# Kernel optimization log

Hardware: AMD Instinct MI355X
Metric: run time of the kernel (lower is better)

Reference implementation:

```python
import jax, jax.numpy as jnp
import numpy as np

N_NODES = 100000
IN_DIM, HID_DIM, OUT_DIM = 1433, 16, 7
N_EDGES = 3200000


def gcn_conv(x, edge_index, W, b, num_nodes):
    # add self loops
    loop = jnp.arange(num_nodes, dtype=edge_index.dtype)
    src = jnp.concatenate([edge_index[0], loop])  # [E+N]
    dst = jnp.concatenate([edge_index[1], loop])
    h = x @ W + b  # [N, out]
    # degree computed on row (edge_index[0]) as in the torch code
    deg = jax.ops.segment_sum(jnp.ones_like(src, dtype=h.dtype), src,
                              num_segments=num_nodes)
    dis = deg ** -0.5  # self-loops guarantee deg >= 1
    norm = dis[src] * dis[dst]  # [E+N]
    msg = norm[:, None] * h[src]  # gather + scale
    return jax.ops.segment_sum(msg, dst, num_segments=num_nodes)  # scatter-add


def setup_inputs() -> dict:
    key = jax.random.key(0)
    k1, k2, k3, k4, k5, k6 = jax.random.split(key, 6)
    x = jax.random.normal(k1, (N_NODES, IN_DIM), dtype=jnp.float32)
    edge_index = jax.random.randint(k2, (2, N_EDGES), 0, N_NODES, dtype=jnp.int64)
    s1 = 1.0 / np.sqrt(IN_DIM)
    s2 = 1.0 / np.sqrt(HID_DIM)
    W1 = jax.random.uniform(k3, (IN_DIM, HID_DIM), jnp.float32, -s1, s1)
    b1 = jax.random.uniform(k4, (HID_DIM,), jnp.float32, -s1, s1)
    W2 = jax.random.uniform(k5, (HID_DIM, OUT_DIM), jnp.float32, -s2, s2)
    b2 = jax.random.uniform(k6, (OUT_DIM,), jnp.float32, -s2, s2)
    return {"x": x, "edge_index": edge_index, "W1": W1, "b1": b1,
            "W2": W2, "b2": b2}


def reference(x, edge_index, W1, b1, W2, b2):
    n = x.shape[0]
    h = gcn_conv(x, edge_index, W1, b1, n)
    h = jax.nn.relu(h)
    # dropout is inactive in eval mode (training=False)
    h = gcn_conv(h, edge_index, W2, b2, n)
    return jax.nn.log_softmax(h, axis=1)
```

## Files before the change

### kernel.cpp

```cpp
#include <hip/hip_runtime.h>
#include <math.h>

constexpr int IN_DIM = 1433;
constexpr int HID    = 16;
constexpr int OUTD   = 7;

__device__ __forceinline__ int edge_get(const int* __restrict__ ei, long long idx, int is64) {
    return is64 ? ei[2 * idx] : ei[idx];
}

__global__ void k_detect_init(const int* __restrict__ ei, int* __restrict__ flag,
                              int* __restrict__ deg, int* __restrict__ cnt, int n) {
    int i = blockIdx.x * blockDim.x + threadIdx.x;
    if (i < n) { deg[i] = 1; cnt[i] = 0; }
    if (blockIdx.x == 0) {
        __shared__ int nzsh;
        if (threadIdx.x == 0) nzsh = 0;
        __syncthreads();
        int nz = 0;
        for (int j = threadIdx.x; j < 2048; j += blockDim.x)
            nz |= (ei[2 * j + 1] != 0) ? 1 : 0;
        if (nz) nzsh = 1;
        __syncthreads();
        if (threadIdx.x == 0) *flag = (nzsh == 0) ? 1 : 0;
    }
}

__global__ __launch_bounds__(128) void k_gemm1h(
        const float* __restrict__ x, const float* __restrict__ W1,
        const float* __restrict__ b1, float* __restrict__ h1, int n,
        const int* __restrict__ ei, int E, const int* __restrict__ flag,
        int* __restrict__ deg, int* __restrict__ cnt, int* __restrict__ packed,
        int nHist) {
    if ((int)blockIdx.x < nHist) {
        int is64 = *flag;
        long long stride = (long long)nHist * blockDim.x;
        for (long long e = (long long)blockIdx.x * blockDim.x + threadIdx.x;
             e < E; e += stride) {
            int s = edge_get(ei, e, is64);
            int d = edge_get(ei, (long long)E + e, is64);
            atomicAdd(&deg[s], 1);
            int slot = atomicAdd(&cnt[d], 1);
            packed[e] = (d << 14) | (slot & 16383);
        }
        return;
    }

    constexpr int BK = 32, XST = 36;
    __shared__ __align__(16) float xs[128 * XST];
    __shared__ __align__(16) float wsm[BK * HID];
    const int t    = threadIdx.x;
    const int c4   = t & 3;
    const int rq   = t >> 2;
    const int row0 = ((int)blockIdx.x - nHist) * 128;

    float xreg[32];
    float wreg[4];
    float4 acc[4];
    #pragma unroll
    for (int j = 0; j < 4; ++j) acc[j] = make_float4(0.f, 0.f, 0.f, 0.f);

    auto issue = [&](int kt) {
        #pragma unroll
        for (int i = 0; i < 32; ++i) {
            int idx  = t + 128 * i;
            int srow = idx >> 5;
            int scol = idx & 31;
            int gr   = row0 + srow;
            int col  = kt + scol;
            float v = 0.f;
            if (gr < n && col < IN_DIM) v = x[(long long)gr * IN_DIM + col];
            xreg[i] = v;
        }
        #pragma unroll
        for (int u = 0; u < 4; ++u) {
            int idx = t + 128 * u;
            int kk  = idx >> 4;
            wreg[u] = (kt + kk < IN_DIM) ? W1[(kt + kk) * HID + (idx & 15)] : 0.f;
        }
    };
    auto commit = [&]() {
        #pragma unroll
        for (int i = 0; i < 32; ++i) {
            int idx  = t + 128 * i;
            int srow = idx >> 5;
            int scol = idx & 31;
            xs[srow * XST + scol] = xreg[i];
        }
        #pragma unroll
        for (int u = 0; u < 4; ++u) wsm[t + 128 * u] = wreg[u];
    };

    const int nkt = (IN_DIM + BK - 1) / BK;
    issue(0);
    for (int it = 0; it < nkt; ++it) {
        commit();
        __syncthreads();
        if (it + 1 < nkt) issue((it + 1) * BK);
        #pragma unroll
        for (int k4 = 0; k4 < BK / 4; ++k4) {
            int k = k4 * 4;
            float4 w0 = *(const float4*)&wsm[(k + 0) * HID + c4 * 4];
            float4 w1 = *(const float4*)&wsm[(k + 1) * HID + c4 * 4];
            float4 w2 = *(const float4*)&wsm[(k + 2) * HID + c4 * 4];
            float4 w3 = *(const float4*)&wsm[(k + 3) * HID + c4 * 4];
            #pragma unroll
            for (int j = 0; j < 4; ++j) {
                float4 xv = *(const float4*)&xs[(rq + 32 * j) * XST + k];
                acc[j].x += xv.x * w0.x + xv.y * w1.x + xv.z * w2.x + xv.w * w3.x;
                acc[j].y += xv.x * w0.y + xv.y * w1.y + xv.z * w2.y + xv.w * w3.y;
                acc[j].z += xv.x * w0.z + xv.y * w1.z + xv.z * w2.z + xv.w * w3.z;
                acc[j].w += xv.x * w0.w + xv.y * w1.w + xv.z * w2.w + xv.w * w3.w;
            }
        }
        __syncthreads();
    }

    float4 bv = *(const float4*)&b1[c4 * 4];
    #pragma unroll
    for (int j = 0; j < 4; ++j) {
        int gr = row0 + rq + 32 * j;
        if (gr < n) {
            float4 hv;
            hv.x = acc[j].x + bv.x;
            hv.y = acc[j].y + bv.y;
            hv.z = acc[j].z + bv.z;
            hv.w = acc[j].w + bv.w;
            *(float4*)&h1[(long long)gr * HID + c4 * 4] = hv;
        }
    }
}

__global__ __launch_bounds__(256) void k_scan1(const int* __restrict__ cnt,
                                               int* __restrict__ bsum,
                                               float* __restrict__ dis, int n) {
    __shared__ int sh[256];
    int t = threadIdx.x;
    int base = blockIdx.x * 1024 + t * 4;
    int s = 0;
    #pragma unroll
    for (int j = 0; j < 4; ++j) {
        int i = base + j;
        if (i < n) {
            s += cnt[i];
            int v = ((const int*)dis)[i];
            dis[i] = rsqrtf((float)v);
        }
    }
    sh[t] = s; __syncthreads();
    for (int o = 128; o > 0; o >>= 1) {
        if (t < o) sh[t] += sh[t + o];
        __syncthreads();
    }
    if (t == 0) bsum[blockIdx.x] = sh[0];
}

__global__ __launch_bounds__(256) void k_scan2(const int* __restrict__ bsum,
                                               int* __restrict__ boff,
                                               int* __restrict__ rp,
                                               int nb, int n, int E) {
    __shared__ int sh[256];
    int t = threadIdx.x;
    int v = (t < nb) ? bsum[t] : 0;
    sh[t] = v; __syncthreads();
    for (int o = 1; o < 256; o <<= 1) {
        int tmp = (t >= o) ? sh[t - o] : 0;
        __syncthreads();
        sh[t] += tmp;
        __syncthreads();
    }
    boff[t] = sh[t] - v;
    if (t == 0) rp[n] = E;
}

__global__ __launch_bounds__(256) void k_scan3(const int* __restrict__ cnt,
                                               const int* __restrict__ boff,
                                               int* __restrict__ rp, int n) {
    __shared__ int sh[256];
    int t = threadIdx.x;
    int base = blockIdx.x * 1024 + t * 4;
    int c[4];
    int s = 0;
    #pragma unroll
    for (int j = 0; j < 4; ++j) {
        int i = base + j;
        c[j] = (i < n) ? cnt[i] : 0;
        s += c[j];
    }
    sh[t] = s; __syncthreads();
    for (int o = 1; o < 256; o <<= 1) {
        int tmp = (t >= o) ? sh[t - o] : 0;
        __syncthreads();
        sh[t] += tmp;
        __syncthreads();
    }
    int run = boff[blockIdx.x] + sh[t] - s;
    #pragma unroll
    for (int j = 0; j < 4; ++j) {
        int i = base + j;
        if (i < n) rp[i] = run;
        run += c[j];
    }
}

__global__ void k_place(const int* __restrict__ ei, int E, const int* __restrict__ flag,
                        const int* __restrict__ packed, const int* __restrict__ rp,
                        int* __restrict__ csr) {
    int e = blockIdx.x * blockDim.x + threadIdx.x;
    if (e >= E) return;
    int is64 = *flag;
    int s  = edge_get(ei, e, is64);
    int p  = packed[e];
    int d  = p >> 14;
    int sl = p & 16383;
    csr[rp[d] + sl] = s;
}

__global__ void k_scale(const float* __restrict__ dis, const float* __restrict__ in,
                        float* __restrict__ out, int n, int squared) {
    int i = blockIdx.x * blockDim.x + threadIdx.x;
    if (i >= n * 4) return;
    int row = i >> 2;
    float d = dis[row];
    if (squared) d *= d;
    float4 v = *(const float4*)&in[(long long)i * 4];
    v.x *= d; v.y *= d; v.z *= d; v.w *= d;
    *(float4*)&out[(long long)i * 4] = v;
}

__global__ __launch_bounds__(256) void k_gather1f(
        const int* __restrict__ rp, const int* __restrict__ csr,
        const float* __restrict__ dis, const float* __restrict__ hs1,
        const float* __restrict__ W2, const float* __restrict__ b2,
        float* __restrict__ hs2, int n) {
    __shared__ float w2s[HID * OUTD];
    __shared__ float b2s[OUTD];
    int t = threadIdx.x;
    if (t < HID * OUTD) w2s[t] = W2[t];
    if (t < OUTD) b2s[t] = b2[t];
    __syncthreads();

    int tid  = blockIdx.x * blockDim.x + t;
    int node = tid >> 2;
    int q    = tid & 3;
    if (node >= n) return;

    float4 acc = *(const float4*)&hs1[(long long)node * HID + q * 4];

    int i = rp[node], end = rp[node + 1];
    for (; i + 4 <= end; i += 4) {
        int s0 = csr[i], s1 = csr[i + 1], s2 = csr[i + 2], s3 = csr[i + 3];
        float4 h0 = *(const float4*)&hs1[(long long)s0 * HID + q * 4];
        float4 h1 = *(const float4*)&hs1[(long long)s1 * HID + q * 4];
        float4 h2 = *(const float4*)&hs1[(long long)s2 * HID + q * 4];
        float4 h3 = *(const float4*)&hs1[(long long)s3 * HID + q * 4];
        acc.x += (h0.x + h1.x) + (h2.x + h3.x);
        acc.y += (h0.y + h1.y) + (h2.y + h3.y);
        acc.z += (h0.z + h1.z) + (h2.z + h3.z);
        acc.w += (h0.w + h1.w) + (h2.w + h3.w);
    }
    for (; i < end; ++i) {
        int s = csr[i];
        float4 h = *(const float4*)&hs1[(long long)s * HID + q * 4];
        acc.x += h.x; acc.y += h.y; acc.z += h.z; acc.w += h.w;
    }

    float dn = dis[node];
    float r0 = fmaxf(dn * acc.x, 0.f), r1 = fmaxf(dn * acc.y, 0.f);
    float r2 = fmaxf(dn * acc.z, 0.f), r3 = fmaxf(dn * acc.w, 0.f);
    float p[OUTD];
    #pragma unroll
    for (int j = 0; j < OUTD; ++j) {
        p[j] = r0 * w2s[(q * 4 + 0) * OUTD + j]
             + r1 * w2s[(q * 4 + 1) * OUTD + j]
             + r2 * w2s[(q * 4 + 2) * OUTD + j]
             + r3 * w2s[(q * 4 + 3) * OUTD + j];
    }
    #pragma unroll
    for (int j = 0; j < OUTD; ++j) {
        p[j] += __shfl_xor(p[j], 1, 4);
        p[j] += __shfl_xor(p[j], 2, 4);
    }
    hs2[(long long)node * OUTD + q] = dn * (p[q] + b2s[q]);
    if (q < 3) hs2[(long long)node * OUTD + q + 4] = dn * (p[q + 4] + b2s[q + 4]);
}

__global__ __launch_bounds__(256) void k_gather2(
        const int* __restrict__ rp, const int* __restrict__ csr,
        const float* __restrict__ dis, const float* __restrict__ hs2,
        float* __restrict__ out, int n) {
    int t = threadIdx.x;
    int node = blockIdx.x * 32 + (t >> 3);
    int q = t & 7;
    if (node >= n) return;
    float acc = -1e30f;
    if (q < OUTD) {
        acc = hs2[(long long)node * OUTD + q];
        int i = rp[node], end = rp[node + 1];
        for (; i + 8 <= end; i += 8) {
            int s0 = csr[i],     s1 = csr[i + 1], s2 = csr[i + 2], s3 = csr[i + 3];
            int s4 = csr[i + 4], s5 = csr[i + 5], s6 = csr[i + 6], s7 = csr[i + 7];
            float v0 = hs2[(long long)s0 * OUTD + q];
            float v1 = hs2[(long long)s1 * OUTD + q];
            float v2 = hs2[(long long)s2 * OUTD + q];
            float v3 = hs2[(long long)s3 * OUTD + q];
            float v4 = hs2[(long long)s4 * OUTD + q];
            float v5 = hs2[(long long)s5 * OUTD + q];
            float v6 = hs2[(long long)s6 * OUTD + q];
            float v7 = hs2[(long long)s7 * OUTD + q];
            acc += ((v0 + v1) + (v2 + v3)) + ((v4 + v5) + (v6 + v7));
        }
        for (; i < end; ++i) {
            int s = csr[i];
            acc += hs2[(long long)s * OUTD + q];
        }
        acc *= dis[node];
    }
    float m = acc;
    #pragma unroll
    for (int o = 1; o < 8; o <<= 1) m = fmaxf(m, __shfl_xor(m, o, 8));
    float ex = (q < OUTD) ? expf(acc - m) : 0.f;
    float ss = ex;
    #pragma unroll
    for (int o = 1; o < 8; o <<= 1) ss += __shfl_xor(ss, o, 8);
    if (q < OUTD) out[(long long)node * OUTD + q] = acc - m - logf(ss);
}

__global__ void k_detect(const int* __restrict__ ei, int* __restrict__ flag) {
    __shared__ int nzsh;
    if (threadIdx.x == 0) nzsh = 0;
    __syncthreads();
    int nz = 0;
    for (int i = threadIdx.x; i < 2048; i += blockDim.x)
        nz |= (ei[2 * i + 1] != 0) ? 1 : 0;
    if (nz) nzsh = 1;
    __syncthreads();
    if (threadIdx.x == 0) *flag = (nzsh == 0) ? 1 : 0;
}

__global__ void k_deg_init(int* __restrict__ deg, int n) {
    int i = blockIdx.x * blockDim.x + threadIdx.x;
    if (i < n) deg[i] = 1;
}

__global__ void k_deg_count(const int* __restrict__ ei, int E,
                            const int* __restrict__ flag, int* __restrict__ deg) {
    int e = blockIdx.x * blockDim.x + threadIdx.x;
    if (e >= E) return;
    int is64 = *flag;
    int s = edge_get(ei, e, is64);
    atomicAdd(&deg[s], 1);
}

__global__ void k_deg_finish(float* __restrict__ dis, int n) {
    int i = blockIdx.x * blockDim.x + threadIdx.x;
    if (i < n) {
        int v = ((const int*)dis)[i];
        dis[i] = rsqrtf((float)v);
    }
}

__global__ void k_agg1(const int* __restrict__ ei, int E, const int* __restrict__ flag,
                       const float* __restrict__ dis, const float* __restrict__ h1,
                       float* __restrict__ a1) {
    long long tid = (long long)blockIdx.x * blockDim.x + threadIdx.x;
    int e = (int)(tid >> 2);
    int q = (int)(tid & 3);
    if (e >= E) return;
    int is64 = *flag;
    int s = edge_get(ei, e, is64);
    int d = edge_get(ei, (long long)E + e, is64);
    float nrm = dis[s] * dis[d];
    float4 v = *(const float4*)&h1[(long long)s * HID + q * 4];
    float* o = &a1[(long long)d * HID + q * 4];
    atomicAdd(o + 0, nrm * v.x);
    atomicAdd(o + 1, nrm * v.y);
    atomicAdd(o + 2, nrm * v.z);
    atomicAdd(o + 3, nrm * v.w);
}

__global__ __launch_bounds__(256) void k_gemm2(
        const float* __restrict__ a1, const float* __restrict__ W2,
        const float* __restrict__ b2, const float* __restrict__ dis,
        float* __restrict__ h2, float* __restrict__ a2, int n) {
    __shared__ float w2s[HID * OUTD];
    __shared__ float b2s[OUTD];
    int t = threadIdx.x;
    if (t < HID * OUTD) w2s[t] = W2[t];
    if (t < OUTD) b2s[t] = b2[t];
    __syncthreads();
    int r = blockIdx.x * blockDim.x + t;
    if (r >= n) return;
    float a[16];
    #pragma unroll
    for (int i = 0; i < 4; ++i) {
        float4 v = *(const float4*)&a1[(long long)r * HID + i * 4];
        a[4 * i + 0] = fmaxf(v.x, 0.f);
        a[4 * i + 1] = fmaxf(v.y, 0.f);
        a[4 * i + 2] = fmaxf(v.z, 0.f);
        a[4 * i + 3] = fmaxf(v.w, 0.f);
    }
    float dd = 0.f;
    if (a2) { float d = dis[r]; dd = d * d; }
    #pragma unroll
    for (int j = 0; j < OUTD; ++j) {
        float acc = b2s[j];
        #pragma unroll
        for (int k = 0; k < HID; ++k) acc += a[k] * w2s[k * OUTD + j];
        h2[(long long)r * OUTD + j] = acc;
        if (a2) a2[(long long)r * OUTD + j] = dd * acc;
    }
}

__global__ void k_agg2(const int* __restrict__ ei, int E, const int* __restrict__ flag,
                       const float* __restrict__ dis, const float* __restrict__ h2,
                       float* __restrict__ a2) {
    long long tid = (long long)blockIdx.x * blockDim.x + threadIdx.x;
    int e = (int)(tid >> 1);
    int q = (int)(tid & 1);
    if (e >= E) return;
    int is64 = *flag;
    int s = edge_get(ei, e, is64);
    int d = edge_get(ei, (long long)E + e, is64);
    float nrm = dis[s] * dis[d];
    int cnt = q ? 3 : 4;
    long long bs = (long long)s * OUTD + q * 4;
    long long bd = (long long)d * OUTD + q * 4;
    #pragma unroll
    for (int j = 0; j < 4; ++j)
        if (j < cnt) atomicAdd(&a2[bd + j], nrm * h2[bs + j]);
}

__global__ void k_lsm(const float* __restrict__ a2, float* __restrict__ out, int n) {
    int r = blockIdx.x * blockDim.x + threadIdx.x;
    if (r >= n) return;
    float v[OUTD];
    #pragma unroll
    for (int j = 0; j < OUTD; ++j) v[j] = a2[(long long)r * OUTD + j];
    float m = v[0];
    #pragma unroll
    for (int j = 1; j < OUTD; ++j) m = fmaxf(m, v[j]);
    float ssum = 0.f;
    #pragma unroll
    for (int j = 0; j < OUTD; ++j) ssum += expf(v[j] - m);
    float l = logf(ssum);
    #pragma unroll
    for (int j = 0; j < OUTD; ++j) out[(long long)r * OUTD + j] = v[j] - m - l;
}

extern "C" void kernel_launch(void* const* d_in, const int* in_sizes, int n_in,
                              void* d_out, int out_size, void* d_ws, size_t ws_size,
                              hipStream_t stream) {
    const float* x  = (const float*)d_in[0];
    const int*   ei = (const int*)d_in[1];
    const float* W1 = (const float*)d_in[2];
    const float* b1 = (const float*)d_in[3];
    const float* W2 = (const float*)d_in[4];
    const float* b2 = (const float*)d_in[5];
    float* out = (float*)d_out;

    const int N = in_sizes[0] / IN_DIM;
    const int E = in_sizes[1] / 2;

    const int TPB = 256;
    const int gN  = (N + TPB - 1) / TPB;
    const int gE  = (E + TPB - 1) / TPB;
    const int gG1 = (N + 127) / 128;
    const int NB  = (N + 1023) / 1024;
    const int nHist = 512;

    float* ws = (float*)d_ws;
    size_t o = 0;
    auto take = [&](size_t cnt) { size_t r = o; o += (cnt + 127) & ~(size_t)127; return r; };

    size_t off_dis  = take((size_t)N);
    size_t off_flag = take(64);
    size_t off_cnt  = take((size_t)N);
    size_t off_rp   = take((size_t)N + 1);
    size_t off_bs   = take(256);
    size_t off_bo   = take(256);
    size_t off_pk   = take((size_t)E);
    size_t off_csr  = take((size_t)E);
    size_t off_h1   = take((size_t)N * HID);
    size_t off_h2   = take((size_t)N * OUTD);
    size_t need_new = o * sizeof(float);

    if (ws_size >= need_new) {
        float* dis  = ws + off_dis;
        int*   degi = (int*)dis;
        int*   flag = (int*)(ws + off_flag);
        int*   cnt  = (int*)(ws + off_cnt);
        int*   rp   = (int*)(ws + off_rp);
        int*   bs   = (int*)(ws + off_bs);
        int*   bo   = (int*)(ws + off_bo);
        int*   pk   = (int*)(ws + off_pk);
        int*   csr  = (int*)(ws + off_csr);
        float* h1   = ws + off_h1;
        float* hs2  = ws + off_h2;

        k_detect_init<<<gN, TPB, 0, stream>>>(ei, flag, degi, cnt, N);
        k_gemm1h<<<nHist + gG1, 128, 0, stream>>>(x, W1, b1, h1, N,
                                                  ei, E, flag, degi, cnt, pk, nHist);
        k_scan1<<<NB, 256, 0, stream>>>(cnt, bs, dis, N);
        k_scan2<<<1, 256, 0, stream>>>(bs, bo, rp, NB, N, E);
        k_scan3<<<NB, 256, 0, stream>>>(cnt, bo, rp, N);
        k_place<<<gE, TPB, 0, stream>>>(ei, E, flag, pk, rp, csr);
        k_scale<<<(int)(((long long)N * 4 + TPB - 1) / TPB), TPB, 0, stream>>>(
            dis, h1, h1, N, 0);
        k_gather1f<<<(int)(((long long)N * 4 + TPB - 1) / TPB), TPB, 0, stream>>>(
            rp, csr, dis, h1, W2, b2, hs2, N);
        k_gather2<<<(N + 31) / 32, 256, 0, stream>>>(rp, csr, dis, hs2, out, N);
    } else {
        o = 0;
        size_t f_dis  = take((size_t)N);
        size_t f_flag = take(64);
        size_t f_h1   = take((size_t)N * HID);
        size_t f_a1   = take((size_t)N * HID);
        size_t f_h2   = take((size_t)N * OUTD);
        size_t f_a2   = take((size_t)N * OUTD);

        float* dis  = ws + f_dis;
        int*   degi = (int*)dis;
        int*   flag = (int*)(ws + f_flag);
        float* h1   = ws + f_h1;
        float* a1   = ws + f_a1;
        float* h2   = ws + f_h2;
        float* a2   = ws + f_a2;

        int g4E = (int)(((long long)4 * E + TPB - 1) / TPB);
        int g2E = (int)(((long long)2 * E + TPB - 1) / TPB);

        k_detect<<<1, 256, 0, stream>>>(ei, flag);
        k_deg_init<<<gN, TPB, 0, stream>>>(degi, N);
        k_deg_count<<<gE, TPB, 0, stream>>>(ei, E, flag, degi);
        k_deg_finish<<<gN, TPB, 0, stream>>>(dis, N);
        k_gemm1h<<<gG1, 128, 0, stream>>>(x, W1, b1, h1, N,
                                          ei, E, flag, nullptr, nullptr, nullptr, 0);
        k_scale<<<(int)(((long long)N * 4 + TPB - 1) / TPB), TPB, 0, stream>>>(
            dis, h1, a1, N, 1);
        k_agg1<<<g4E, TPB, 0, stream>>>(ei, E, flag, dis, h1, a1);
        k_gemm2<<<gN, TPB, 0, stream>>>(a1, W2, b2, dis, h2, a2, N);
        k_agg2<<<g2E, TPB, 0, stream>>>(ei, E, flag, dis, h2, a2);
        k_lsm<<<gN, TPB, 0, stream>>>(a2, out, N);
    }
}
```

Measured before the change: 668.1 us.

## Split histogram out of GEMM kernel and fuse degree scaling into GEMM epilogue

The edge histogram, which used to run in dedicated blocks inside the first GEMM launch, becomes its own kernel. The GEMM now runs after the degree scan so it can multiply its output by dis directly, which removes the separate k_scale pass over h1. This gives up the overlap between the atomic-heavy histogram and the bandwidth-heavy GEMM, in exchange for one fewer elementwise kernel and less h1 traffic. The fallback path also folds its scaling into the GEMM epilogue.

```diff
diff --git a/kernel.cpp b/kernel.cpp
--- a/kernel.cpp
+++ b/kernel.cpp
@@ -26,33 +26,115 @@
     }
 }
 
-__global__ __launch_bounds__(128) void k_gemm1h(
+__global__ void k_hist2(const int* __restrict__ ei, int E, const int* __restrict__ flag,
+                        int* __restrict__ deg, int* __restrict__ cnt,
+                        int* __restrict__ packed) {
+    int e = blockIdx.x * blockDim.x + threadIdx.x;
+    if (e >= E) return;
+    int is64 = *flag;
+    int s = edge_get(ei, e, is64);
+    int d = edge_get(ei, (long long)E + e, is64);
+    atomicAdd(&deg[s], 1);
+    int slot = atomicAdd(&cnt[d], 1);
+    packed[e] = (d << 14) | (slot & 16383);
+}
+
+__global__ __launch_bounds__(256) void k_scan1(const int* __restrict__ cnt,
+                                               int* __restrict__ bsum,
+                                               float* __restrict__ dis, int n) {
+    __shared__ int sh[256];
+    int t = threadIdx.x;
+    int base = blockIdx.x * 1024 + t * 4;
+    int s = 0;
+    #pragma unroll
+    for (int j = 0; j < 4; ++j) {
+        int i = base + j;
+        if (i < n) {
+            s += cnt[i];
+            int v = ((const int*)dis)[i];
+            dis[i] = rsqrtf((float)v);
+        }
+    }
+    sh[t] = s; __syncthreads();
+    for (int o = 128; o > 0; o >>= 1) {
+        if (t < o) sh[t] += sh[t + o];
+        __syncthreads();
+    }
+    if (t == 0) bsum[blockIdx.x] = sh[0];
+}
+
+__global__ __launch_bounds__(256) void k_scan2(const int* __restrict__ bsum,
+                                               int* __restrict__ boff,
+                                               int* __restrict__ rp,
+                                               int nb, int n, int E) {
+    __shared__ int sh[256];
+    int t = threadIdx.x;
+    int v = (t < nb) ? bsum[t] : 0;
+    sh[t] = v; __syncthreads();
+    for (int o = 1; o < 256; o <<= 1) {
+        int tmp = (t >= o) ? sh[t - o] : 0;
+        __syncthreads();
+        sh[t] += tmp;
+        __syncthreads();
+    }
+    boff[t] = sh[t] - v;
+    if (t == 0) rp[n] = E;
+}
+
+__global__ __launch_bounds__(256) void k_scan3(const int* __restrict__ cnt,
+                                               const int* __restrict__ boff,
+                                               int* __restrict__ rp, int n) {
+    __shared__ int sh[256];
+    int t = threadIdx.x;
+    int base = blockIdx.x * 1024 + t * 4;
+    int c[4];
+    int s = 0;
+    #pragma unroll
+    for (int j = 0; j < 4; ++j) {
+        int i = base + j;
+        c[j] = (i < n) ? cnt[i] : 0;
+        s += c[j];
+    }
+    sh[t] = s; __syncthreads();
+    for (int o = 1; o < 256; o <<= 1) {
+        int tmp = (t >= o) ? sh[t - o] : 0;
+        __syncthreads();
+        sh[t] += tmp;
+        __syncthreads();
+    }
+    int run = boff[blockIdx.x] + sh[t] - s;
+    #pragma unroll
+    for (int j = 0; j < 4; ++j) {
+        int i = base + j;
+        if (i < n) rp[i] = run;
+        run += c[j];
+    }
+}
+
+__global__ void k_place(const int* __restrict__ ei, int E, const int* __restrict__ flag,
+                        const int* __restrict__ packed, const int* __restrict__ rp,
+                        int* __restrict__ csr) {
+    int e = blockIdx.x * blockDim.x + threadIdx.x;
+    if (e >= E) return;
+    int is64 = *flag;
+    int s  = edge_get(ei, e, is64);
+    int p  = packed[e];
+    int d  = p >> 14;
+    int sl = p & 16383;
+    csr[rp[d] + sl] = s;
+}
+
+__global__ __launch_bounds__(128) void k_gemm1(
         const float* __restrict__ x, const float* __restrict__ W1,
-        const float* __restrict__ b1, float* __restrict__ h1, int n,
-        const int* __restrict__ ei, int E, const int* __restrict__ flag,
-        int* __restrict__ deg, int* __restrict__ cnt, int* __restrict__ packed,
-        int nHist) {
-    if ((int)blockIdx.x < nHist) {
-        int is64 = *flag;
-        long long stride = (long long)nHist * blockDim.x;
-        for (long long e = (long long)blockIdx.x * blockDim.x + threadIdx.x;
-             e < E; e += stride) {
-            int s = edge_get(ei, e, is64);
-            int d = edge_get(ei, (long long)E + e, is64);
-            atomicAdd(&deg[s], 1);
-            int slot = atomicAdd(&cnt[d], 1);
-            packed[e] = (d << 14) | (slot & 16383);
-        }
-        return;
-    }
-
+        const float* __restrict__ b1, const float* __restrict__ dis,
+        float* __restrict__ h1, float* __restrict__ a1, int n, int scale_out) {
     constexpr int BK = 32, XST = 36;
     __shared__ __align__(16) float xs[128 * XST];
     __shared__ __align__(16) float wsm[BK * HID];
     const int t    = threadIdx.x;
     const int c4   = t & 3;
     const int rq   = t >> 2;
-    const int row0 = ((int)blockIdx.x - nHist) * 128;
+    const int row0 = blockIdx.x * 128;
 
     float xreg[32];
     float wreg[4];
@@ -126,94 +208,20 @@
             hv.y = acc[j].y + bv.y;
             hv.z = acc[j].z + bv.z;
             hv.w = acc[j].w + bv.w;
+            if (scale_out) {
+                float d = dis[gr];
+                hv.x *= d; hv.y *= d; hv.z *= d; hv.w *= d;
+            }
             *(float4*)&h1[(long long)gr * HID + c4 * 4] = hv;
-        }
-    }
-}
-
-__global__ __launch_bounds__(256) void k_scan1(const int* __restrict__ cnt,
-                                               int* __restrict__ bsum,
-                                               float* __restrict__ dis, int n) {
-    __shared__ int sh[256];
-    int t = threadIdx.x;
-    int base = blockIdx.x * 1024 + t * 4;
-    int s = 0;
-    #pragma unroll
-    for (int j = 0; j < 4; ++j) {
-        int i = base + j;
-        if (i < n) {
-            s += cnt[i];
-            int v = ((const int*)dis)[i];
-            dis[i] = rsqrtf((float)v);
-        }
-    }
-    sh[t] = s; __syncthreads();
-    for (int o = 128; o > 0; o >>= 1) {
-        if (t < o) sh[t] += sh[t + o];
-        __syncthreads();
-    }
-    if (t == 0) bsum[blockIdx.x] = sh[0];
-}
-
-__global__ __launch_bounds__(256) void k_scan2(const int* __restrict__ bsum,
-                                               int* __restrict__ boff,
-                                               int* __restrict__ rp,
-                                               int nb, int n, int E) {
-    __shared__ int sh[256];
-    int t = threadIdx.x;
-    int v = (t < nb) ? bsum[t] : 0;
-    sh[t] = v; __syncthreads();
-    for (int o = 1; o < 256; o <<= 1) {
-        int tmp = (t >= o) ? sh[t - o] : 0;
-        __syncthreads();
-        sh[t] += tmp;
-        __syncthreads();
-    }
-    boff[t] = sh[t] - v;
-    if (t == 0) rp[n] = E;
-}
-
-__global__ __launch_bounds__(256) void k_scan3(const int* __restrict__ cnt,
-                                               const int* __restrict__ boff,
-                                               int* __restrict__ rp, int n) {
-    __shared__ int sh[256];
-    int t = threadIdx.x;
-    int base = blockIdx.x * 1024 + t * 4;
-    int c[4];
-    int s = 0;
-    #pragma unroll
-    for (int j = 0; j < 4; ++j) {
-        int i = base + j;
-        c[j] = (i < n) ? cnt[i] : 0;
-        s += c[j];
-    }
-    sh[t] = s; __syncthreads();
-    for (int o = 1; o < 256; o <<= 1) {
-        int tmp = (t >= o) ? sh[t - o] : 0;
-        __syncthreads();
-        sh[t] += tmp;
-        __syncthreads();
-    }
-    int run = boff[blockIdx.x] + sh[t] - s;
-    #pragma unroll
-    for (int j = 0; j < 4; ++j) {
-        int i = base + j;
-        if (i < n) rp[i] = run;
-        run += c[j];
-    }
-}
-
-__global__ void k_place(const int* __restrict__ ei, int E, const int* __restrict__ flag,
-                        const int* __restrict__ packed, const int* __restrict__ rp,
-                        int* __restrict__ csr) {
-    int e = blockIdx.x * blockDim.x + threadIdx.x;
-    if (e >= E) return;
-    int is64 = *flag;
-    int s  = edge_get(ei, e, is64);
-    int p  = packed[e];
-    int d  = p >> 14;
-    int sl = p & 16383;
-    csr[rp[d] + sl] = s;
+            if (a1) {
+                float d = dis[gr];
+                float dd = d * d;
+                float4 av;
+                av.x = dd * hv.x; av.y = dd * hv.y; av.z = dd * hv.z; av.w = dd * hv.w;
+                *(float4*)&a1[(long long)gr * HID + c4 * 4] = av;
+            }
+        }
+    }
 }
 
 __global__ void k_scale(const float* __restrict__ dis, const float* __restrict__ in,
@@ -467,7 +475,6 @@
     const int gE  = (E + TPB - 1) / TPB;
     const int gG1 = (N + 127) / 128;
     const int NB  = (N + 1023) / 1024;
-    const int nHist = 512;
 
     float* ws = (float*)d_ws;
     size_t o = 0;
@@ -495,20 +502,18 @@
         int*   bo   = (int*)(ws + off_bo);
         int*   pk   = (int*)(ws + off_pk);
         int*   csr  = (int*)(ws + off_csr);
-        float* h1   = ws + off_h1;
+        float* hs1  = ws + off_h1;
         float* hs2  = ws + off_h2;
 
         k_detect_init<<<gN, TPB, 0, stream>>>(ei, flag, degi, cnt, N);
-        k_gemm1h<<<nHist + gG1, 128, 0, stream>>>(x, W1, b1, h1, N,
-                                                  ei, E, flag, degi, cnt, pk, nHist);
+        k_hist2<<<gE, TPB, 0, stream>>>(ei, E, flag, degi, cnt, pk);
         k_scan1<<<NB, 256, 0, stream>>>(cnt, bs, dis, N);
         k_scan2<<<1, 256, 0, stream>>>(bs, bo, rp, NB, N, E);
         k_scan3<<<NB, 256, 0, stream>>>(cnt, bo, rp, N);
+        k_gemm1<<<gG1, 128, 0, stream>>>(x, W1, b1, dis, hs1, nullptr, N, 1);
         k_place<<<gE, TPB, 0, stream>>>(ei, E, flag, pk, rp, csr);
-        k_scale<<<(int)(((long long)N * 4 + TPB - 1) / TPB), TPB, 0, stream>>>(
-            dis, h1, h1, N, 0);
         k_gather1f<<<(int)(((long long)N * 4 + TPB - 1) / TPB), TPB, 0, stream>>>(
-            rp, csr, dis, h1, W2, b2, hs2, N);
+            rp, csr, dis, hs1, W2, b2, hs2, N);
         k_gather2<<<(N + 31) / 32, 256, 0, stream>>>(rp, csr, dis, hs2, out, N);
     } else {
         o = 0;
@@ -534,10 +539,7 @@
         k_deg_init<<<gN, TPB, 0, stream>>>(degi, N);
         k_deg_count<<<gE, TPB, 0, stream>>>(ei, E, flag, degi);
         k_deg_finish<<<gN, TPB, 0, stream>>>(dis, N);
-        k_gemm1h<<<gG1, 128, 0, stream>>>(x, W1, b1, h1, N,
-                                          ei, E, flag, nullptr, nullptr, nullptr, 0);
-        k_scale<<<(int)(((long long)N * 4 + TPB - 1) / TPB), TPB, 0, stream>>>(
-            dis, h1, a1, N, 1);
+        k_gemm1<<<gG1, 128, 0, stream>>>(x, W1, b1, dis, h1, a1, N, 0);
         k_agg1<<<g4E, TPB, 0, stream>>>(ei, E, flag, dis, h1, a1);
         k_gemm2<<<gN, TPB, 0, stream>>>(a1, W2, b2, dis, h2, a2, N);
         k_agg2<<<g2E, TPB, 0, stream>>>(ei, E, flag, dis, h2, a2);
```

Measured after the change: 687.5 us. 1.03x slower.
